# Kernel optimization log

Measured on AMD Instinct MI355X. Metric: run time of the kernel, lower is better.

Reference implementation:

```python
import jax, jax.numpy as jnp
import numpy as np

B, C, H, W, P, D, NH = 16, 3, 512, 512, 16, 128, 4
GH, GW = H // P, W // P
NP_ = GH * GW            # 1024 total patches
PD = C * P * P           # 768 patch dim
NV = NP_ // 4            # 256 visible tokens (mask_ratio = 0.75)
ENC_L, DEC_L = 6, 2
FF = 4 * D

def layer_norm(x, w, b, eps=1e-5):
    m = jnp.mean(x, -1, keepdims=True)
    v = jnp.mean((x - m) ** 2, -1, keepdims=True)
    return (x - m) * jax.lax.rsqrt(v + eps) * w + b

def mha(x, qkv_w, qkv_b, out_w, out_b):
    Bq, S, Dm = x.shape
    hd = Dm // NH
    q, k, v = jnp.split(x @ qkv_w.T + qkv_b, 3, axis=-1)
    sh = lambda t: t.reshape(Bq, S, NH, hd).transpose(0, 2, 1, 3)
    q, k, v = sh(q), sh(k), sh(v)
    scale = jnp.asarray(1.0 / np.sqrt(hd), x.dtype)
    att = jax.nn.softmax(jnp.einsum('bhqd,bhkd->bhqk', q, k) * scale, axis=-1)
    o = jnp.einsum('bhqk,bhkd->bhqd', att, v).transpose(0, 2, 1, 3).reshape(Bq, S, Dm)
    return o @ out_w.T + out_b

def stack(x, qkv_w, qkv_b, out_w, out_b, ln1_w, ln1_b, ff1_w, ff1_b, ff2_w, ff2_b, ln2_w, ln2_b):
    # post-norm nn.TransformerEncoderLayer, eval mode (dropout off), exact gelu
    for i in range(qkv_w.shape[0]):
        x = layer_norm(x + mha(x, qkv_w[i], qkv_b[i], out_w[i], out_b[i]), ln1_w[i], ln1_b[i])
        h = jax.nn.gelu(x @ ff1_w[i].T + ff1_b[i], approximate=False) @ ff2_w[i].T + ff2_b[i]
        x = layer_norm(x + h, ln2_w[i], ln2_b[i])
    return x

def setup_inputs():
    key = jax.random.key(0)
    ks = iter(jax.random.split(key, 64))
    f = lambda *s: jax.random.normal(next(ks), s, jnp.float32) * 0.02
    inp = {
        'x': jax.random.normal(next(ks), (B, C, H, W), jnp.float32),
        'vis_idx': jax.vmap(lambda k: jax.random.permutation(k, NP_))(jax.random.split(next(ks), B))[:, :NV].astype(jnp.int32),
        'w_patch': f(D, PD), 'b_patch': jnp.zeros((D,), jnp.float32),
        'mask_token': f(1, D), 'pos_embed': f(1, NP_, D),
        'w_recon': f(PD, D), 'b_recon': jnp.zeros((PD,), jnp.float32),
    }
    for pre, L in (('enc', ENC_L), ('dec', DEC_L)):
        inp[pre + '_qkv_w'] = f(L, 3 * D, D)
        inp[pre + '_qkv_b'] = jnp.zeros((L, 3 * D), jnp.float32)
        inp[pre + '_out_w'] = f(L, D, D)
        inp[pre + '_out_b'] = jnp.zeros((L, D), jnp.float32)
        inp[pre + '_ln1_w'] = jnp.ones((L, D), jnp.float32)
        inp[pre + '_ln1_b'] = jnp.zeros((L, D), jnp.float32)
        inp[pre + '_ff1_w'] = f(L, FF, D)
        inp[pre + '_ff1_b'] = jnp.zeros((L, FF), jnp.float32)
        inp[pre + '_ff2_w'] = f(L, D, FF)
        inp[pre + '_ff2_b'] = jnp.zeros((L, D), jnp.float32)
        inp[pre + '_ln2_w'] = jnp.ones((L, D), jnp.float32)
        inp[pre + '_ln2_b'] = jnp.zeros((L, D), jnp.float32)
    return inp

def reference(x, vis_idx, w_patch, b_patch, mask_token, pos_embed, w_recon, b_recon,
              enc_qkv_w, enc_qkv_b, enc_out_w, enc_out_b, enc_ln1_w, enc_ln1_b,
              enc_ff1_w, enc_ff1_b, enc_ff2_w, enc_ff2_b, enc_ln2_w, enc_ln2_b,
              dec_qkv_w, dec_qkv_b, dec_out_w, dec_out_b, dec_ln1_w, dec_ln1_b,
              dec_ff1_w, dec_ff1_b, dec_ff2_w, dec_ff2_b, dec_ln2_w, dec_ln2_b):
    # patchify: matches nn.Unfold(kernel=stride=P) channel-major patch layout
    patches = x.reshape(B, C, GH, P, GW, P).transpose(0, 2, 4, 1, 3, 5).reshape(B, NP_, PD)
    tok = patches @ w_patch.T + b_patch                    # [B, NP, D]
    bidx = jnp.arange(B)[:, None]
    vis = tok[bidx, vis_idx]                               # [B, NV, D] packed visible tokens
    enc = stack(vis, enc_qkv_w, enc_qkv_b, enc_out_w, enc_out_b, enc_ln1_w, enc_ln1_b,
                enc_ff1_w, enc_ff1_b, enc_ff2_w, enc_ff2_b, enc_ln2_w, enc_ln2_b)
    # mask_token everywhere, scatter encoded tokens back to their positions
    full = jnp.broadcast_to(mask_token, (B, NP_, D)).at[bidx, vis_idx].set(enc)
    full = full + pos_embed
    dec = stack(full, dec_qkv_w, dec_qkv_b, dec_out_w, dec_out_b, dec_ln1_w, dec_ln1_b,
                dec_ff1_w, dec_ff1_b, dec_ff2_w, dec_ff2_b, dec_ln2_w, dec_ln2_b)
    rec = dec @ w_recon.T + b_recon                        # [B, NP, PD]
    # unpatchify: [B,GH,GW,C,P,P] -> permute(0,3,1,4,2,5) -> [B,C,H,W]
    img = rec.reshape(B, GH, GW, C, P, P).transpose(0, 3, 1, 4, 2, 5).reshape(B, C, H, W)
    return img
```

## Files before the change

kernel.cpp:

```cpp
#include <hip/hip_runtime.h>
#include <math.h>

typedef unsigned short ushort_t;
typedef __attribute__((ext_vector_type(8))) short bf16x8;
typedef __attribute__((ext_vector_type(4))) float f32x4;
typedef __attribute__((ext_vector_type(16))) float f32x16;
typedef __attribute__((ext_vector_type(2))) unsigned uint2v;

__device__ __forceinline__ ushort_t f2bf(float f){
  union{float f; unsigned u;} v; v.f = f;
  unsigned r = v.u + 0x7FFFu + ((v.u >> 16) & 1u);
  return (ushort_t)(r >> 16);
}
__device__ __forceinline__ float bf2f(ushort_t h){
  union{unsigned u; float f;} v; v.u = ((unsigned)h) << 16; return v.f;
}
__device__ __forceinline__ float gelu_exact(float v){
  return 0.5f * v * (1.f + erff(v * 0.70710678118654752f));
}
#define GLD16(gp, lp) __builtin_amdgcn_global_load_lds( \
    (const __attribute__((address_space(1))) void*)(gp), \
    (__attribute__((address_space(3))) void*)(lp), 16, 0, 0)

static __device__ __forceinline__ f32x4 mfma16(bf16x8 a, bf16x8 b, f32x4 c){
  return __builtin_amdgcn_mfma_f32_16x16x32_bf16(a, b, c, 0, 0, 0);
}
static __device__ __forceinline__ f32x16 mfma32(bf16x8 a, bf16x8 b, f32x16 c){
  return __builtin_amdgcn_mfma_f32_32x32x16_bf16(a, b, c, 0, 0, 0);
}

template<int BT, int MI, int SRC, int EPI>
__global__ __launch_bounds__(256) void mfma_gemm(
    const ushort_t* __restrict__ A, const ushort_t* __restrict__ W,
    const float* __restrict__ bias, void* __restrict__ Cout,
    int M, int N, int K, ushort_t* __restrict__ vT, int slog, float qs)
{
  __shared__ ushort_t smem[BT*64 + BT*64];
  ushort_t* Al = smem;
  ushort_t* Wl = smem + BT*64;
  const int tid = threadIdx.x;
  const int lane = tid & 63, w = tid >> 6;
  const int wr = w >> 1, wc = w & 1;
  const int g = lane >> 4, lq = lane & 15;
  const int m0 = blockIdx.y * BT, n0 = blockIdx.x * BT;

  const f32x4 zf = {0.f, 0.f, 0.f, 0.f};
  f32x4 acc[MI][MI];
#pragma unroll
  for (int i = 0; i < MI; ++i)
#pragma unroll
    for (int j = 0; j < MI; ++j) acc[i][j] = zf;

  float bv[MI];
#pragma unroll
  for (int ni = 0; ni < MI; ++ni) bv[ni] = bias[n0 + wc*(BT/2) + ni*16 + lq];

  const int KT = K >> 6;
  for (int kt = 0; kt < KT; ++kt) {
    if (kt) __syncthreads();
    const int k0 = kt << 6;
#pragma unroll
    for (int i = 0; i < BT/32; ++i) {
      int chunk = i*256 + tid;
      int row = chunk >> 3, c = chunk & 7;
      int kk = k0 + ((c ^ (row & 7)) << 3);
      const ushort_t* src;
      if (SRC == 0) {
        src = A + (size_t)(m0 + row) * K + kk;
      } else {
        int gm = m0 + row;
        int bb = gm >> 10, pp = gm & 1023, gh = pp >> 5, gw = pp & 31;
        int ci = kk >> 8, rem = kk & 255, py = rem >> 4, px = rem & 15;
        src = A + ((size_t)((bb*3 + ci)*512 + gh*16 + py) * 512 + gw*16 + px);
      }
      GLD16(src, (char*)Al + chunk*16);
    }
#pragma unroll
    for (int i = 0; i < BT/32; ++i) {
      int chunk = i*256 + tid;
      int row = chunk >> 3, c = chunk & 7;
      int kk = k0 + ((c ^ (row & 7)) << 3);
      GLD16(W + (size_t)(n0 + row) * K + kk, (char*)Wl + chunk*16);
    }
    __syncthreads();
#pragma unroll
    for (int ks = 0; ks < 2; ++ks) {
      bf16x8 af[MI], bfr[MI];
#pragma unroll
      for (int mi = 0; mi < MI; ++mi) {
        int row = wr*(BT/2) + mi*16 + lq;
        int c = (ks*4 + g) ^ (row & 7);
        af[mi] = *(const bf16x8*)((const char*)Al + row*128 + c*16);
      }
#pragma unroll
      for (int ni = 0; ni < MI; ++ni) {
        int row = wc*(BT/2) + ni*16 + lq;
        int c = (ks*4 + g) ^ (row & 7);
        bfr[ni] = *(const bf16x8*)((const char*)Wl + row*128 + c*16);
      }
#pragma unroll
      for (int mi = 0; mi < MI; ++mi)
#pragma unroll
        for (int ni = 0; ni < MI; ++ni)
          acc[mi][ni] = mfma16(af[mi], bfr[ni], acc[mi][ni]);
    }
  }

  if (EPI == 3 && n0 >= 256) {
    const int Sm1 = (1 << slog) - 1;
#pragma unroll
    for (int mi = 0; mi < MI; ++mi) {
      int gm0 = m0 + wr*(BT/2) + mi*16 + g*4;
      int bb = gm0 >> slog, s0 = gm0 & Sm1;
#pragma unroll
      for (int ni = 0; ni < MI; ++ni) {
        int n = n0 + wc*(BT/2) + ni*16 + lq;
        int vcol = n - 256, hh = vcol >> 5, dd = vcol & 31;
        unsigned pw0 = ((unsigned)f2bf(acc[mi][ni][0] + bv[ni])) |
                       (((unsigned)f2bf(acc[mi][ni][1] + bv[ni])) << 16);
        unsigned pw1 = ((unsigned)f2bf(acc[mi][ni][2] + bv[ni])) |
                       (((unsigned)f2bf(acc[mi][ni][3] + bv[ni])) << 16);
        uint2 pk; pk.x = pw0; pk.y = pw1;
        *(uint2*)(vT + (((size_t)(bb*4 + hh)*32 + dd) << slog) + s0) = pk;
      }
    }
    return;
  }

  if (EPI == 2) {
    float* img = (float*)Cout;
#pragma unroll
    for (int mi = 0; mi < MI; ++mi) {
#pragma unroll
      for (int r = 0; r < 4; ++r) {
        int gm = m0 + wr*(BT/2) + mi*16 + g*4 + r;
        int bb = gm >> 10, pp = gm & 1023, gh = pp >> 5, gw = pp & 31;
#pragma unroll
        for (int ni = 0; ni < MI; ++ni) {
          int n = n0 + wc*(BT/2) + ni*16 + lq;
          int ci = n >> 8, rem = n & 255, py = rem >> 4, px = rem & 15;
          img[(size_t)((bb*3 + ci)*512 + gh*16 + py)*512 + gw*16 + px] =
              acc[mi][ni][r] + bv[ni];
        }
      }
    }
  } else {
    const float cs = (EPI == 3 && n0 < 128) ? qs : 1.0f;
    __syncthreads();
    constexpr int CPR = BT/8;
#pragma unroll
    for (int mi = 0; mi < MI; ++mi)
#pragma unroll
      for (int ni = 0; ni < MI; ++ni)
#pragma unroll
        for (int r = 0; r < 4; ++r) {
          int row = wr*(BT/2) + mi*16 + g*4 + r;
          int col = wc*(BT/2) + ni*16 + lq;
          float v = acc[mi][ni][r] + bv[ni];
          if (EPI == 3) v *= cs;
          int cc = (col >> 3) ^ (row & (CPR-1));
          smem[row*BT + cc*8 + (col & 7)] = f2bf(v);
        }
    __syncthreads();
    ushort_t* Co = (ushort_t*)Cout;
#pragma unroll
    for (int i = 0; i < BT*BT/2048; ++i) {
      int chunk = i*256 + tid;
      int row = chunk / CPR, cc = chunk % CPR;
      int c = cc ^ (row & (CPR-1));
      bf16x8 v = *(const bf16x8*)((const char*)smem + chunk*16);
      *(bf16x8*)(Co + (size_t)(m0+row)*N + n0 + c*8) = v;
    }
  }
}

template<int MI2, int QKV>
__global__ __launch_bounds__(512, 4) void mega8(
    const ushort_t* __restrict__ Ao, const ushort_t* __restrict__ Wo,
    const float* __restrict__ bo, ushort_t* __restrict__ X,
    const float* __restrict__ l1w, const float* __restrict__ l1b,
    const ushort_t* __restrict__ W1, const float* __restrict__ b1,
    const ushort_t* __restrict__ W2, const float* __restrict__ b2,
    const float* __restrict__ l2w, const float* __restrict__ l2b,
    const ushort_t* __restrict__ Wq, const float* __restrict__ bq,
    ushort_t* __restrict__ qkvb, ushort_t* __restrict__ vT,
    int slog, float qs)
{
  constexpr int BM = MI2 * 16;
  constexpr int TB = BM * 128;
  __shared__ __align__(16) ushort_t Xl[2*BM*64];
  __shared__ __align__(16) ushort_t Hl[8*BM*64];
  __shared__ __align__(16) float red[2][BM][8];
  const int tid = threadIdx.x, lane = tid & 63, w = tid >> 6;
  const int g = lane >> 4, lq = lane & 15;
  const int m0 = blockIdx.x * BM;
  const int col0 = w*16 + lq;
  const f32x4 zf = {0.f,0.f,0.f,0.f};

  f32x4 acc[MI2];
#pragma unroll
  for (int mi = 0; mi < MI2; ++mi) acc[mi] = zf;
  {
    bf16x8 a1[MI2][4], bo8[4];
#pragma unroll
    for (int mi = 0; mi < MI2; ++mi)
#pragma unroll
      for (int kf = 0; kf < 4; ++kf)
        a1[mi][kf] = *(const bf16x8*)(Ao + (size_t)(m0 + mi*16 + lq)*128 + kf*32 + g*8);
#pragma unroll
    for (int kf = 0; kf < 4; ++kf)
      bo8[kf] = *(const bf16x8*)(Wo + (size_t)col0*128 + kf*32 + g*8);
#pragma unroll
    for (int kf = 0; kf < 4; ++kf)
#pragma unroll
      for (int mi = 0; mi < MI2; ++mi)
        acc[mi] = mfma16(a1[mi][kf], bo8[kf], acc[mi]);
  }

  float xp[MI2][4];
  {
    const float bv = bo[col0], lwv = l1w[col0], lbv = l1b[col0];
#pragma unroll
    for (int mi = 0; mi < MI2; ++mi)
#pragma unroll
      for (int r = 0; r < 4; ++r) {
        int row = m0 + mi*16 + g*4 + r;
        float v = acc[mi][r] + bv + bf2f(X[(size_t)row*128 + col0]);
        xp[mi][r] = v;
        float s = v, q = v*v;
        s += __shfl_xor(s,1); s += __shfl_xor(s,2); s += __shfl_xor(s,4); s += __shfl_xor(s,8);
        q += __shfl_xor(q,1); q += __shfl_xor(q,2); q += __shfl_xor(q,4); q += __shfl_xor(q,8);
        if (lq == 0) { red[0][mi*16+g*4+r][w] = s; red[1][mi*16+g*4+r][w] = q; }
      }
    __syncthreads();
#pragma unroll
    for (int mi = 0; mi < MI2; ++mi)
#pragma unroll
      for (int r = 0; r < 4; ++r) {
        int rl = mi*16 + g*4 + r;
        float4 s0 = *(const float4*)&red[0][rl][0], s1 = *(const float4*)&red[0][rl][4];
        float4 q0 = *(const float4*)&red[1][rl][0], q1 = *(const float4*)&red[1][rl][4];
        float s = s0.x+s0.y+s0.z+s0.w + s1.x+s1.y+s1.z+s1.w;
        float q = q0.x+q0.y+q0.z+q0.w + q1.x+q1.y+q1.z+q1.w;
        float mean = s * 0.0078125f;
        float var = q * 0.0078125f - mean*mean;
        float rstd = rsqrtf(var + 1e-5f);
        float val = (xp[mi][r]-mean)*rstd*lwv + lbv;
        xp[mi][r] = val;
        ushort_t hv = f2bf(val);
        X[(size_t)(m0+rl)*128 + col0] = hv;
        int kt = col0 >> 6, c8 = (col0 & 63) >> 3, he = col0 & 7;
        *(ushort_t*)((char*)Xl + kt*TB + rl*128 + ((c8 ^ (rl & 7)) << 4) + he*2) = hv;
      }
  }
  __syncthreads();

  bf16x8 a2[MI2][4];
#pragma unroll
  for (int mi = 0; mi < MI2; ++mi)
#pragma unroll
    for (int kf = 0; kf < 4; ++kf) {
      int kt = kf >> 1, row = mi*16 + lq;
      int c = ((kf & 1)*4 + g) ^ (row & 7);
      a2[mi][kf] = *(const bf16x8*)((const char*)Xl + kt*TB + row*128 + c*16);
    }

#pragma unroll
  for (int hp = 0; hp < 4; ++hp) {
    const int hid = hp*128 + col0;
    bf16x8 b18[4];
#pragma unroll
    for (int kf = 0; kf < 4; ++kf)
      b18[kf] = *(const bf16x8*)(W1 + (size_t)hid*128 + kf*32 + g*8);
    f32x4 acc1[MI2];
#pragma unroll
    for (int mi = 0; mi < MI2; ++mi) acc1[mi] = zf;
#pragma unroll
    for (int kf = 0; kf < 4; ++kf)
#pragma unroll
      for (int mi = 0; mi < MI2; ++mi)
        acc1[mi] = mfma16(a2[mi][kf], b18[kf], acc1[mi]);
    const float bb = b1[hid];
    const int hkt = hid >> 6, hc8 = (hid & 63) >> 3, he = hid & 7;
#pragma unroll
    for (int mi = 0; mi < MI2; ++mi)
#pragma unroll
      for (int r = 0; r < 4; ++r) {
        int mrow = mi*16 + g*4 + r;
        float hv = gelu_exact(acc1[mi][r] + bb);
        *(ushort_t*)((char*)Hl + hkt*TB + mrow*128 + ((hc8 ^ (mrow & 7)) << 4) + he*2) = f2bf(hv);
      }
  }
  __syncthreads();

  f32x4 acc2[MI2];
#pragma unroll
  for (int mi = 0; mi < MI2; ++mi) acc2[mi] = zf;
#pragma unroll
  for (int kf = 0; kf < 16; ++kf) {
    int kt = kf >> 1;
    bf16x8 af[MI2], bfr;
#pragma unroll
    for (int mi = 0; mi < MI2; ++mi) {
      int row = mi*16 + lq;
      int c = ((kf & 1)*4 + g) ^ (row & 7);
      af[mi] = *(const bf16x8*)((const char*)Hl + kt*TB + row*128 + c*16);
    }
    bfr = *(const bf16x8*)(W2 + (size_t)col0*512 + kf*32 + g*8);
#pragma unroll
    for (int mi = 0; mi < MI2; ++mi)
      acc2[mi] = mfma16(af[mi], bfr, acc2[mi]);
  }

  {
    const float bv = b2[col0], lwv = l2w[col0], lbv = l2b[col0];
#pragma unroll
    for (int mi = 0; mi < MI2; ++mi)
#pragma unroll
      for (int r = 0; r < 4; ++r) {
        float v = acc2[mi][r] + bv + xp[mi][r];
        xp[mi][r] = v;
        float s = v, q = v*v;
        s += __shfl_xor(s,1); s += __shfl_xor(s,2); s += __shfl_xor(s,4); s += __shfl_xor(s,8);
        q += __shfl_xor(q,1); q += __shfl_xor(q,2); q += __shfl_xor(q,4); q += __shfl_xor(q,8);
        if (lq == 0) { red[0][mi*16+g*4+r][w] = s; red[1][mi*16+g*4+r][w] = q; }
      }
    __syncthreads();
#pragma unroll
    for (int mi = 0; mi < MI2; ++mi)
#pragma unroll
      for (int r = 0; r < 4; ++r) {
        int rl = mi*16 + g*4 + r;
        float4 s0 = *(const float4*)&red[0][rl][0], s1 = *(const float4*)&red[0][rl][4];
        float4 q0 = *(const float4*)&red[1][rl][0], q1 = *(const float4*)&red[1][rl][4];
        float s = s0.x+s0.y+s0.z+s0.w + s1.x+s1.y+s1.z+s1.w;
        float q = q0.x+q0.y+q0.z+q0.w + q1.x+q1.y+q1.z+q1.w;
        float mean = s * 0.0078125f;
        float var = q * 0.0078125f - mean*mean;
        float rstd = rsqrtf(var + 1e-5f);
        float val = (xp[mi][r]-mean)*rstd*lwv + lbv;
        ushort_t hv = f2bf(val);
        X[(size_t)(m0+rl)*128 + col0] = hv;
        if (QKV) {
          int kt = col0 >> 6, c8 = (col0 & 63) >> 3, he = col0 & 7;
          *(ushort_t*)((char*)Xl + kt*TB + rl*128 + ((c8 ^ (rl & 7)) << 4) + he*2) = hv;
        }
      }
  }

  if (QKV) {
    __syncthreads();
    bf16x8 a3[MI2][4];
#pragma unroll
    for (int mi = 0; mi < MI2; ++mi)
#pragma unroll
      for (int kf = 0; kf < 4; ++kf) {
        int kt = kf >> 1, row = mi*16 + lq;
        int c = ((kf & 1)*4 + g) ^ (row & 7);
        a3[mi][kf] = *(const bf16x8*)((const char*)Xl + kt*TB + row*128 + c*16);
      }
    const int Sm1 = (1 << slog) - 1;
#pragma unroll
    for (int pp = 0; pp < 3; ++pp) {
      const int colq = pp*128 + col0;
      bf16x8 bq8[4];
#pragma unroll
      for (int kf = 0; kf < 4; ++kf)
        bq8[kf] = *(const bf16x8*)(Wq + (size_t)colq*128 + kf*32 + g*8);
      f32x4 aq[MI2];
#pragma unroll
      for (int mi = 0; mi < MI2; ++mi) aq[mi] = zf;
#pragma unroll
      for (int kf = 0; kf < 4; ++kf)
#pragma unroll
        for (int mi = 0; mi < MI2; ++mi)
          aq[mi] = mfma16(a3[mi][kf], bq8[kf], aq[mi]);
      const float bias = bq[colq];
      if (pp < 2) {
        const float sc = (pp == 0) ? qs : 1.f;
#pragma unroll
        for (int mi = 0; mi < MI2; ++mi)
#pragma unroll
          for (int r = 0; r < 4; ++r) {
            int row = m0 + mi*16 + g*4 + r;
            qkvb[(size_t)row*384 + colq] = f2bf((aq[mi][r] + bias)*sc);
          }
      } else {
        const int hh = col0 >> 5, dd = col0 & 31;
#pragma unroll
        for (int mi = 0; mi < MI2; ++mi) {
          int gm0 = m0 + mi*16 + g*4;
          int bb = gm0 >> slog, s0 = gm0 & Sm1;
          unsigned pw0 = ((unsigned)f2bf(aq[mi][0] + bias)) |
                         (((unsigned)f2bf(aq[mi][1] + bias)) << 16);
          unsigned pw1 = ((unsigned)f2bf(aq[mi][2] + bias)) |
                         (((unsigned)f2bf(aq[mi][3] + bias)) << 16);
          uint2 pk; pk.x = pw0; pk.y = pw1;
          *(uint2*)(vT + (((size_t)(bb*4 + hh)*32 + dd) << slog) + s0) = pk;
        }
      }
    }
  }
}

template<int S, int JS>
__global__ __launch_bounds__(256) void attn32(
    const ushort_t* __restrict__ qkv, const ushort_t* __restrict__ vTg,
    ushort_t* __restrict__ o)
{
  constexpr int LDSB = (JS == 1) ? 16384 : 32768;
  __shared__ __align__(16) char smem[LDSB];
  const int tid = threadIdx.x, lane = tid & 63, w = tid >> 6;
  const int hi = lane >> 5, lq = lane & 31;
  int lin = blockIdx.x;
  int nid = (lin & 7) * 64 + (lin >> 3);
  int bx = nid & 7, bh = nid >> 3;
  int h = bh & 3, b = bh >> 2;
  const int q0 = (JS == 1) ? (bx*128 + w*32) : (bx*32);

  bf16x8 bq0 = *(const bf16x8*)(qkv + (size_t)(b*S + q0 + lq)*384 + h*32 + hi*8);
  bf16x8 bq1 = *(const bf16x8*)(qkv + (size_t)(b*S + q0 + lq)*384 + h*32 + 16 + hi*8);

  f32x16 O;
#pragma unroll
  for (int i = 0; i < 16; ++i) O[i] = 0.f;
  const f32x16 z16 = O;
  float l = 0.f;

  auto stageK = [&](char* Kb, int j0, int ci){
    int k = ci >> 2, cp = ci & 3, c = cp ^ (k & 3);
    GLD16(qkv + (size_t)(b*S + j0 + k)*384 + 128 + h*32 + c*8, Kb + ci*16);
  };
  auto stageV = [&](char* Vb, int j0, int ci){
    int d = ci >> 3, cp = ci & 7, c = cp ^ (d & 7);
    GLD16(vTg + (size_t)(bh*32 + d)*S + j0 + c*8, Vb + ci*16);
  };

  auto sm_pack = [&](const f32x16& stv, unsigned* wd){
    float p[16];
#pragma unroll
    for (int r = 0; r < 16; ++r) { p[r] = __expf(stv[r]); l += p[r]; }
#pragma unroll
    for (int i = 0; i < 8; ++i) {
      unsigned u0 = __float_as_uint(p[2*i])   + 0x8000u;
      unsigned u1 = __float_as_uint(p[2*i+1]) + 0x8000u;
      wd[i] = (u0 >> 16) | (u1 & 0xFFFF0000u);
    }
  };
  auto pvstep = [&](unsigned* wd, const char* Vb, int mt){
    uint2v s02 = __builtin_amdgcn_permlane32_swap(wd[0], wd[2], false, false);
    uint2v s13 = __builtin_amdgcn_permlane32_swap(wd[1], wd[3], false, false);
    uint2v s46 = __builtin_amdgcn_permlane32_swap(wd[4], wd[6], false, false);
    uint2v s57 = __builtin_amdgcn_permlane32_swap(wd[5], wd[7], false, false);
    union { unsigned u[4]; bf16x8 v; } pa0, pa1;
    pa0.u[0] = s02[0]; pa0.u[1] = s13[0]; pa0.u[2] = s02[1]; pa0.u[3] = s13[1];
    pa1.u[0] = s46[0]; pa1.u[1] = s57[0]; pa1.u[2] = s46[1]; pa1.u[3] = s57[1];
    int d = lq;
    bf16x8 v0 = *(const bf16x8*)(Vb + d*128 + (((mt*4 + hi)     ^ (d & 7)) << 4));
    bf16x8 v1 = *(const bf16x8*)(Vb + d*128 + (((mt*4 + 2 + hi) ^ (d & 7)) << 4));
    O = mfma32(pa0.v, v0, O);
    O = mfma32(pa1.v, v1, O);
  };
  auto computeTile = [&](const char* Kb, const char* Vb){
    const int k0 = lq, k1 = 32 + lq;
    bf16x8 a00 = *(const bf16x8*)(Kb + k0*64 + (((hi)     ^ (k0 & 3)) << 4));
    bf16x8 a01 = *(const bf16x8*)(Kb + k0*64 + (((2 + hi) ^ (k0 & 3)) << 4));
    f32x16 st0 = mfma32(a00, bq0, z16);
    st0 = mfma32(a01, bq1, st0);
    bf16x8 a10 = *(const bf16x8*)(Kb + k1*64 + (((hi)     ^ (k1 & 3)) << 4));
    bf16x8 a11 = *(const bf16x8*)(Kb + k1*64 + (((2 + hi) ^ (k1 & 3)) << 4));
    f32x16 st1 = mfma32(a10, bq0, z16);
    st1 = mfma32(a11, bq1, st1);
    unsigned wd0[8], wd1[8];
    sm_pack(st0, wd0);
    sm_pack(st1, wd1);
    pvstep(wd0, Vb, 0);
    pvstep(wd1, Vb, 1);
  };

  if (JS == 4) {
    char* Kb = smem + w*8192;
    char* Vb = Kb + 4096;
    const int j0 = w*64;
#pragma unroll
    for (int i = 0; i < 4; ++i) stageK(Kb, j0, i*64 + lane);
#pragma unroll
    for (int i = 0; i < 4; ++i) stageV(Vb, j0, i*64 + lane);
    __syncthreads();
    computeTile(Kb, Vb);
    float lw = l + __shfl_xor(l, 32);
    __syncthreads();
    float* F = (float*)smem;
#pragma unroll
    for (int r = 0; r < 16; ++r) F[(w*16 + r)*64 + lane] = O[r];
    if (hi == 0) F[4096 + w*32 + lq] = lw;
    __syncthreads();
    if (w == 0) {
      float lt = F[4096 + lq] + F[4096 + 32 + lq] + F[4096 + 64 + lq] + F[4096 + 96 + lq];
      float linv = 1.f / lt;
#pragma unroll
      for (int r = 0; r < 16; ++r) {
        float s = F[r*64 + lane] + F[(16 + r)*64 + lane] +
                  F[(32 + r)*64 + lane] + F[(48 + r)*64 + lane];
        int qr = (r & 3) + 8*(r >> 2) + 4*hi;
        float li = __shfl(linv, qr);
        o[(size_t)(b*S + q0 + qr)*128 + h*32 + lq] = f2bf(s*li);
      }
    }
  } else {
    char* K0 = smem, *V0 = smem + 4096, *K1 = smem + 8192, *V1 = smem + 12288;
    stageK(K0, 0, tid);
    stageV(V0, 0, tid);
    const int NT = S/64;
    for (int t = 0; t < NT; ++t) {
      __syncthreads();
      if (t + 1 < NT) {
        char* Kb = (t & 1) ? K0 : K1;
        char* Vb = (t & 1) ? V0 : V1;
        stageK(Kb, (t + 1)*64, tid);
        stageV(Vb, (t + 1)*64, tid);
      }
      computeTile((t & 1) ? K1 : K0, (t & 1) ? V1 : V0);
    }
    float ltot = l + __shfl_xor(l, 32);
    float linv = 1.f / ltot;
#pragma unroll
    for (int r = 0; r < 16; ++r) {
      int qr = (r & 3) + 8*(r >> 2) + 4*hi;
      float li = __shfl(linv, qr);
      o[(size_t)(b*S + q0 + qr)*128 + h*32 + lq] = f2bf(O[r]*li);
    }
  }
}

struct CastArgs {
  const float* src[11];
  ushort_t* dst[11];
  int start[11];
};
__global__ __launch_bounds__(256) void cast_all(CastArgs a, int total8){
  int i = blockIdx.x*256 + threadIdx.x;
  if (i >= total8) return;
  int s = 0;
#pragma unroll
  for (int k = 1; k < 11; ++k) if (i >= a.start[k]) s = k;
  int off = (i - a.start[s]) * 8;
  const float* sp = a.src[s] + off;
  float4 f0 = *(const float4*)sp;
  float4 f1 = *(const float4*)(sp + 4);
  bf16x8 r;
  r[0]=(short)f2bf(f0.x); r[1]=(short)f2bf(f0.y); r[2]=(short)f2bf(f0.z); r[3]=(short)f2bf(f0.w);
  r[4]=(short)f2bf(f1.x); r[5]=(short)f2bf(f1.y); r[6]=(short)f2bf(f1.z); r[7]=(short)f2bf(f1.w);
  *(bf16x8*)(a.dst[s] + off) = r;
}

__global__ __launch_bounds__(256) void gather_k(const ushort_t* __restrict__ tok,
    const int* __restrict__ vis, ushort_t* __restrict__ xe){
  int i = blockIdx.x*256 + threadIdx.x;
  int r = i >> 4, e = (i & 15)*8;
  int b = r >> 8;
  int p = vis[r];
  *(bf16x8*)(xe + (size_t)r*128 + e) = *(const bf16x8*)(tok + ((size_t)b*1024 + p)*128 + e);
}

__global__ __launch_bounds__(256) void fill_k(const float* __restrict__ mask_tok,
    const float* __restrict__ pos, ushort_t* __restrict__ full){
  int i = blockIdx.x*256 + threadIdx.x;
  int off0 = i*8;
  int d = off0 & 127;
  int p = (off0 >> 7) & 1023;
  float4 m0 = *(const float4*)(mask_tok + d);
  float4 m1 = *(const float4*)(mask_tok + d + 4);
  const float* pp = pos + (size_t)p*128 + d;
  float4 p0 = *(const float4*)pp, p1 = *(const float4*)(pp + 4);
  bf16x8 r;
  r[0]=(short)f2bf(m0.x+p0.x); r[1]=(short)f2bf(m0.y+p0.y);
  r[2]=(short)f2bf(m0.z+p0.z); r[3]=(short)f2bf(m0.w+p0.w);
  r[4]=(short)f2bf(m1.x+p1.x); r[5]=(short)f2bf(m1.y+p1.y);
  r[6]=(short)f2bf(m1.z+p1.z); r[7]=(short)f2bf(m1.w+p1.w);
  *(bf16x8*)(full + off0) = r;
}

__global__ __launch_bounds__(256) void scatter_k(const ushort_t* __restrict__ enc,
    const int* __restrict__ vis, const float* __restrict__ pos, ushort_t* __restrict__ full){
  int i = blockIdx.x*256 + threadIdx.x;
  int r = i >> 4, e = (i & 15)*8;
  int b = r >> 8;
  int p = vis[r];
  bf16x8 ev = *(const bf16x8*)(enc + (size_t)r*128 + e);
  const float* pp = pos + (size_t)p*128 + e;
  float4 p0 = *(const float4*)pp, p1 = *(const float4*)(pp + 4);
  bf16x8 out;
  out[0]=(short)f2bf(bf2f((ushort_t)ev[0]) + p0.x);
  out[1]=(short)f2bf(bf2f((ushort_t)ev[1]) + p0.y);
  out[2]=(short)f2bf(bf2f((ushort_t)ev[2]) + p0.z);
  out[3]=(short)f2bf(bf2f((ushort_t)ev[3]) + p0.w);
  out[4]=(short)f2bf(bf2f((ushort_t)ev[4]) + p1.x);
  out[5]=(short)f2bf(bf2f((ushort_t)ev[5]) + p1.y);
  out[6]=(short)f2bf(bf2f((ushort_t)ev[6]) + p1.z);
  out[7]=(short)f2bf(bf2f((ushort_t)ev[7]) + p1.w);
  *(bf16x8*)(full + ((size_t)b*1024 + p)*128 + e) = out;
}

extern "C" void kernel_launch(void* const* d_in, const int* in_sizes, int n_in,
                              void* d_out, int out_size, void* d_ws, size_t ws_size,
                              hipStream_t stream)
{
  const float* x        = (const float*)d_in[0];
  const int*   vis      = (const int*)d_in[1];
  const float* b_patch  = (const float*)d_in[3];
  const float* mask_tok = (const float*)d_in[4];
  const float* pos      = (const float*)d_in[5];
  const float* b_recon  = (const float*)d_in[7];
  float* out = (float*)d_out;
  const float QS = 0.17677669529663687f;

  ushort_t* ws    = (ushort_t*)d_ws;
  ushort_t* tok   = ws;
  ushort_t* xe    = tok  + 2097152;
  ushort_t* qkvb  = xe   + 524288;
  ushort_t* obuf  = qkvb + 8388608;
  ushort_t* tbuf  = obuf + 2097152;
  ushort_t* xbf   = tbuf + 2097152;
  ushort_t* wbf   = xbf  + 12582912;

  ushort_t* w_qkv_e = wbf;
  ushort_t* w_out_e = w_qkv_e + 294912;
  ushort_t* w_ff1_e = w_out_e + 98304;
  ushort_t* w_ff2_e = w_ff1_e + 393216;
  ushort_t* w_qkv_d = w_ff2_e + 393216;
  ushort_t* w_out_d = w_qkv_d + 98304;
  ushort_t* w_ff1_d = w_out_d + 32768;
  ushort_t* w_ff2_d = w_ff1_d + 131072;
  ushort_t* w_pat   = w_ff2_d + 131072;
  ushort_t* w_rec   = w_pat   + 98304;
  ushort_t* vT      = w_rec   + 98304;

  CastArgs ca;
  const float* srcs[11] = {x, (const float*)d_in[8], (const float*)d_in[10],
                           (const float*)d_in[14], (const float*)d_in[16],
                           (const float*)d_in[20], (const float*)d_in[22],
                           (const float*)d_in[26], (const float*)d_in[28],
                           (const float*)d_in[2], (const float*)d_in[6]};
  ushort_t* dsts[11] = {xbf, w_qkv_e, w_out_e, w_ff1_e, w_ff2_e,
                        w_qkv_d, w_out_d, w_ff1_d, w_ff2_d, w_pat, w_rec};
  int sizes[11] = {12582912, 294912, 98304, 393216, 393216,
                   98304, 32768, 131072, 131072, 98304, 98304};
  int acc8 = 0;
  for (int k = 0; k < 11; ++k){ ca.src[k]=srcs[k]; ca.dst[k]=dsts[k]; ca.start[k]=acc8; acc8 += sizes[k]/8; }
  cast_all<<<dim3((acc8 + 255)/256), 256, 0, stream>>>(ca, acc8);

  mfma_gemm<64,2,1,0><<<dim3(2,256), 256, 0, stream>>>(xbf, w_pat, b_patch, tok, 16384, 128, 768, nullptr, 0, 1.f);
  gather_k<<<dim3(256), 256, 0, stream>>>(tok, vis, xe);

  mfma_gemm<64,2,0,3><<<dim3(6,64), 256, 0, stream>>>(xe, w_qkv_e, (const float*)d_in[9], qkvb, 4096, 384, 128, vT, 8, QS);
  for (int L = 0; L < 6; ++L) {
    const float* ob  = (const float*)d_in[11] + L*128;
    const float* l1w = (const float*)d_in[12] + L*128;
    const float* l1b = (const float*)d_in[13] + L*128;
    const float* f1b = (const float*)d_in[15] + L*512;
    const float* f2b = (const float*)d_in[17] + L*128;
    const float* l2w = (const float*)d_in[18] + L*128;
    const float* l2b = (const float*)d_in[19] + L*128;
    attn32<256,4><<<dim3(512), 256, 0, stream>>>(qkvb, vT, obuf);
    if (L < 5) {
      mega8<1,1><<<dim3(256), 512, 0, stream>>>(obuf, w_out_e + L*16384, ob, xe,
          l1w, l1b, w_ff1_e + L*65536, f1b, w_ff2_e + L*65536, f2b, l2w, l2b,
          w_qkv_e + (L+1)*49152, (const float*)d_in[9] + (L+1)*384, qkvb, vT, 8, QS);
    } else {
      mega8<1,0><<<dim3(256), 512, 0, stream>>>(obuf, w_out_e + L*16384, ob, xe,
          l1w, l1b, w_ff1_e + L*65536, f1b, w_ff2_e + L*65536, f2b, l2w, l2b,
          w_qkv_e, (const float*)d_in[9], qkvb, vT, 8, QS);
    }
  }

  fill_k<<<dim3(1024), 256, 0, stream>>>(mask_tok, pos, tok);
  scatter_k<<<dim3(256), 256, 0, stream>>>(xe, vis, pos, tok);

  mfma_gemm<128,4,0,3><<<dim3(3,128), 256, 0, stream>>>(tok, w_qkv_d, (const float*)d_in[21], qkvb, 16384, 384, 128, vT, 10, QS);
  for (int L = 0; L < 2; ++L) {
    const float* ob  = (const float*)d_in[23] + L*128;
    const float* l1w = (const float*)d_in[24] + L*128;
    const float* l1b = (const float*)d_in[25] + L*128;
    const float* f1b = (const float*)d_in[27] + L*512;
    const float* f2b = (const float*)d_in[29] + L*128;
    const float* l2w = (const float*)d_in[30] + L*128;
    const float* l2b = (const float*)d_in[31] + L*128;
    attn32<1024,1><<<dim3(512), 256, 0, stream>>>(qkvb, vT, obuf);
    if (L < 1) {
      mega8<2,1><<<dim3(512), 512, 0, stream>>>(obuf, w_out_d + L*16384, ob, tok,
          l1w, l1b, w_ff1_d + L*65536, f1b, w_ff2_d + L*65536, f2b, l2w, l2b,
          w_qkv_d + 49152, (const float*)d_in[21] + 384, qkvb, vT, 10, QS);
    } else {
      mega8<2,0><<<dim3(512), 512, 0, stream>>>(obuf, w_out_d + L*16384, ob, tok,
          l1w, l1b, w_ff1_d + L*65536, f1b, w_ff2_d + L*65536, f2b, l2w, l2b,
          w_qkv_d, (const float*)d_in[21], qkvb, vT, 10, QS);
    }
  }

  mfma_gemm<128,4,0,2><<<dim3(6,128), 256, 0, stream>>>(tok, w_rec, b_recon, out, 16384, 768, 128, nullptr, 0, 1.f);
}
```

Before: 330.9 us.

## Prefetch fused-layer weights into registers and use fast erf approximation

Restructures the fused out-proj/LN/FFN/LN/QKV kernel so weight fragments for W1, W2 and the next QKV projection, the residual values and the bias/LN parameters are loaded into registers ahead of use, overlapping global latency with earlier MFMA work. The residual X write after LN1 is dropped. __syncthreads is replaced by an LDS-only waitcnt plus barrier. Exact erff in GELU is swapped for an Abramowitz-Stegun polynomial with max error around 1e-7, which is cheaper but slightly changes numerics. Holding many bf16x8 fragments at once raises register pressure and may reduce occupancy or cause spills.

```diff
diff --git a/kernel.cpp b/kernel.cpp
--- a/kernel.cpp
+++ b/kernel.cpp
@@ -18,9 +18,26 @@
 __device__ __forceinline__ float gelu_exact(float v){
   return 0.5f * v * (1.f + erff(v * 0.70710678118654752f));
 }
+__device__ __forceinline__ float erf_fast(float x){
+  float ax = fabsf(x);
+  float t = 1.f / fmaf(0.3275911f, ax, 1.f);
+  float y = t*fmaf(t, fmaf(t, fmaf(t, fmaf(t, 1.061405429f, -1.453152027f),
+            1.421413741f), -0.284496736f), 0.254829592f);
+  float r = 1.f - y * __expf(-ax*ax);
+  return copysignf(r, x);
+}
+__device__ __forceinline__ float gelu_fast(float v){
+  return 0.5f * v * (1.f + erf_fast(v * 0.70710678118654752f));
+}
 #define GLD16(gp, lp) __builtin_amdgcn_global_load_lds( \
     (const __attribute__((address_space(1))) void*)(gp), \
     (__attribute__((address_space(3))) void*)(lp), 16, 0, 0)
+
+#define BAR_LDS() do { \
+  asm volatile("s_waitcnt lgkmcnt(0)" ::: "memory"); \
+  __builtin_amdgcn_s_barrier(); \
+  asm volatile("" ::: "memory"); \
+} while (0)
 
 static __device__ __forceinline__ f32x4 mfma16(bf16x8 a, bf16x8 b, f32x4 c){
   return __builtin_amdgcn_mfma_f32_16x16x32_bf16(a, b, c, 0, 0, 0);
@@ -197,63 +214,79 @@
   const int col0 = w*16 + lq;
   const f32x4 zf = {0.f,0.f,0.f,0.f};
 
+  bf16x8 a1[MI2][4], bo8[4];
+#pragma unroll
+  for (int mi = 0; mi < MI2; ++mi)
+#pragma unroll
+    for (int kf = 0; kf < 4; ++kf)
+      a1[mi][kf] = *(const bf16x8*)(Ao + (size_t)(m0 + mi*16 + lq)*128 + kf*32 + g*8);
+#pragma unroll
+  for (int kf = 0; kf < 4; ++kf)
+    bo8[kf] = *(const bf16x8*)(Wo + (size_t)col0*128 + kf*32 + g*8);
+  ushort_t rsv[MI2][4];
+#pragma unroll
+  for (int mi = 0; mi < MI2; ++mi)
+#pragma unroll
+    for (int r = 0; r < 4; ++r)
+      rsv[mi][r] = X[(size_t)(m0 + mi*16 + g*4 + r)*128 + col0];
+  bf16x8 w1p[4][4];
+#pragma unroll
+  for (int hp = 0; hp < 2; ++hp)
+#pragma unroll
+    for (int kf = 0; kf < 4; ++kf)
+      w1p[hp][kf] = *(const bf16x8*)(W1 + (size_t)(hp*128 + col0)*128 + kf*32 + g*8);
+  const float bo_v = bo[col0], l1w_v = l1w[col0], l1b_v = l1b[col0];
+  const float b2_v = b2[col0], l2w_v = l2w[col0], l2b_v = l2b[col0];
+  float b1_v[4];
+#pragma unroll
+  for (int hp = 0; hp < 4; ++hp) b1_v[hp] = b1[hp*128 + col0];
+
   f32x4 acc[MI2];
 #pragma unroll
   for (int mi = 0; mi < MI2; ++mi) acc[mi] = zf;
-  {
-    bf16x8 a1[MI2][4], bo8[4];
+#pragma unroll
+  for (int kf = 0; kf < 4; ++kf)
 #pragma unroll
     for (int mi = 0; mi < MI2; ++mi)
-#pragma unroll
-      for (int kf = 0; kf < 4; ++kf)
-        a1[mi][kf] = *(const bf16x8*)(Ao + (size_t)(m0 + mi*16 + lq)*128 + kf*32 + g*8);
+      acc[mi] = mfma16(a1[mi][kf], bo8[kf], acc[mi]);
+
+#pragma unroll
+  for (int hp = 2; hp < 4; ++hp)
 #pragma unroll
     for (int kf = 0; kf < 4; ++kf)
-      bo8[kf] = *(const bf16x8*)(Wo + (size_t)col0*128 + kf*32 + g*8);
-#pragma unroll
-    for (int kf = 0; kf < 4; ++kf)
-#pragma unroll
-      for (int mi = 0; mi < MI2; ++mi)
-        acc[mi] = mfma16(a1[mi][kf], bo8[kf], acc[mi]);
-  }
+      w1p[hp][kf] = *(const bf16x8*)(W1 + (size_t)(hp*128 + col0)*128 + kf*32 + g*8);
 
   float xp[MI2][4];
-  {
-    const float bv = bo[col0], lwv = l1w[col0], lbv = l1b[col0];
-#pragma unroll
-    for (int mi = 0; mi < MI2; ++mi)
-#pragma unroll
-      for (int r = 0; r < 4; ++r) {
-        int row = m0 + mi*16 + g*4 + r;
-        float v = acc[mi][r] + bv + bf2f(X[(size_t)row*128 + col0]);
-        xp[mi][r] = v;
-        float s = v, q = v*v;
-        s += __shfl_xor(s,1); s += __shfl_xor(s,2); s += __shfl_xor(s,4); s += __shfl_xor(s,8);
-        q += __shfl_xor(q,1); q += __shfl_xor(q,2); q += __shfl_xor(q,4); q += __shfl_xor(q,8);
-        if (lq == 0) { red[0][mi*16+g*4+r][w] = s; red[1][mi*16+g*4+r][w] = q; }
-      }
-    __syncthreads();
-#pragma unroll
-    for (int mi = 0; mi < MI2; ++mi)
-#pragma unroll
-      for (int r = 0; r < 4; ++r) {
-        int rl = mi*16 + g*4 + r;
-        float4 s0 = *(const float4*)&red[0][rl][0], s1 = *(const float4*)&red[0][rl][4];
-        float4 q0 = *(const float4*)&red[1][rl][0], q1 = *(const float4*)&red[1][rl][4];
-        float s = s0.x+s0.y+s0.z+s0.w + s1.x+s1.y+s1.z+s1.w;
-        float q = q0.x+q0.y+q0.z+q0.w + q1.x+q1.y+q1.z+q1.w;
-        float mean = s * 0.0078125f;
-        float var = q * 0.0078125f - mean*mean;
-        float rstd = rsqrtf(var + 1e-5f);
-        float val = (xp[mi][r]-mean)*rstd*lwv + lbv;
-        xp[mi][r] = val;
-        ushort_t hv = f2bf(val);
-        X[(size_t)(m0+rl)*128 + col0] = hv;
-        int kt = col0 >> 6, c8 = (col0 & 63) >> 3, he = col0 & 7;
-        *(ushort_t*)((char*)Xl + kt*TB + rl*128 + ((c8 ^ (rl & 7)) << 4) + he*2) = hv;
-      }
-  }
-  __syncthreads();
+#pragma unroll
+  for (int mi = 0; mi < MI2; ++mi)
+#pragma unroll
+    for (int r = 0; r < 4; ++r) {
+      float v = acc[mi][r] + bo_v + bf2f(rsv[mi][r]);
+      xp[mi][r] = v;
+      float s = v, q = v*v;
+      s += __shfl_xor(s,1); s += __shfl_xor(s,2); s += __shfl_xor(s,4); s += __shfl_xor(s,8);
+      q += __shfl_xor(q,1); q += __shfl_xor(q,2); q += __shfl_xor(q,4); q += __shfl_xor(q,8);
+      if (lq == 0) { red[0][mi*16+g*4+r][w] = s; red[1][mi*16+g*4+r][w] = q; }
+    }
+  BAR_LDS();
+#pragma unroll
+  for (int mi = 0; mi < MI2; ++mi)
+#pragma unroll
+    for (int r = 0; r < 4; ++r) {
+      int rl = mi*16 + g*4 + r;
+      float4 s0 = *(const float4*)&red[0][rl][0], s1 = *(const float4*)&red[0][rl][4];
+      float4 q0 = *(const float4*)&red[1][rl][0], q1 = *(const float4*)&red[1][rl][4];
+      float s = s0.x+s0.y+s0.z+s0.w + s1.x+s1.y+s1.z+s1.w;
+      float q = q0.x+q0.y+q0.z+q0.w + q1.x+q1.y+q1.z+q1.w;
+      float mean = s * 0.0078125f;
+      float var = q * 0.0078125f - mean*mean;
+      float rstd = rsqrtf(var + 1e-5f);
+      float val = (xp[mi][r]-mean)*rstd*l1w_v + l1b_v;
+      xp[mi][r] = val;
+      int kt = col0 >> 6, c8 = (col0 & 63) >> 3, he = col0 & 7;
+      *(ushort_t*)((char*)Xl + kt*TB + rl*128 + ((c8 ^ (rl & 7)) << 4) + he*2) = f2bf(val);
+    }
+  BAR_LDS();
 
   bf16x8 a2[MI2][4];
 #pragma unroll
@@ -265,91 +298,102 @@
       a2[mi][kf] = *(const bf16x8*)((const char*)Xl + kt*TB + row*128 + c*16);
     }
 
+  bf16x8 w2p[16];
 #pragma unroll
   for (int hp = 0; hp < 4; ++hp) {
+    f32x4 acc1[MI2];
+#pragma unroll
+    for (int mi = 0; mi < MI2; ++mi) acc1[mi] = zf;
+#pragma unroll
+    for (int kf = 0; kf < 4; ++kf)
+#pragma unroll
+      for (int mi = 0; mi < MI2; ++mi)
+        acc1[mi] = mfma16(a2[mi][kf], w1p[hp][kf], acc1[mi]);
+#pragma unroll
+    for (int j = 0; j < 4; ++j)
+      w2p[hp*4 + j] = *(const bf16x8*)(W2 + (size_t)col0*512 + (hp*4 + j)*32 + g*8);
     const int hid = hp*128 + col0;
-    bf16x8 b18[4];
-#pragma unroll
-    for (int kf = 0; kf < 4; ++kf)
-      b18[kf] = *(const bf16x8*)(W1 + (size_t)hid*128 + kf*32 + g*8);
-    f32x4 acc1[MI2];
-#pragma unroll
-    for (int mi = 0; mi < MI2; ++mi) acc1[mi] = zf;
-#pragma unroll
-    for (int kf = 0; kf < 4; ++kf)
-#pragma unroll
-      for (int mi = 0; mi < MI2; ++mi)
-        acc1[mi] = mfma16(a2[mi][kf], b18[kf], acc1[mi]);
-    const float bb = b1[hid];
     const int hkt = hid >> 6, hc8 = (hid & 63) >> 3, he = hid & 7;
 #pragma unroll
     for (int mi = 0; mi < MI2; ++mi)
 #pragma unroll
       for (int r = 0; r < 4; ++r) {
         int mrow = mi*16 + g*4 + r;
-        float hv = gelu_exact(acc1[mi][r] + bb);
+        float hv = gelu_fast(acc1[mi][r] + b1_v[hp]);
         *(ushort_t*)((char*)Hl + hkt*TB + mrow*128 + ((hc8 ^ (mrow & 7)) << 4) + he*2) = f2bf(hv);
       }
   }
-  __syncthreads();
-
+  BAR_LDS();
+
+  bf16x8 wqp[3][4];
   f32x4 acc2[MI2];
 #pragma unroll
   for (int mi = 0; mi < MI2; ++mi) acc2[mi] = zf;
 #pragma unroll
   for (int kf = 0; kf < 16; ++kf) {
     int kt = kf >> 1;
-    bf16x8 af[MI2], bfr;
+    bf16x8 af[MI2];
 #pragma unroll
     for (int mi = 0; mi < MI2; ++mi) {
       int row = mi*16 + lq;
       int c = ((kf & 1)*4 + g) ^ (row & 7);
       af[mi] = *(const bf16x8*)((const char*)Hl + kt*TB + row*128 + c*16);
     }
-    bfr = *(const bf16x8*)(W2 + (size_t)col0*512 + kf*32 + g*8);
 #pragma unroll
     for (int mi = 0; mi < MI2; ++mi)
-      acc2[mi] = mfma16(af[mi], bfr, acc2[mi]);
-  }
-
-  {
-    const float bv = b2[col0], lwv = l2w[col0], lbv = l2b[col0];
-#pragma unroll
-    for (int mi = 0; mi < MI2; ++mi)
-#pragma unroll
-      for (int r = 0; r < 4; ++r) {
-        float v = acc2[mi][r] + bv + xp[mi][r];
-        xp[mi][r] = v;
-        float s = v, q = v*v;
-        s += __shfl_xor(s,1); s += __shfl_xor(s,2); s += __shfl_xor(s,4); s += __shfl_xor(s,8);
-        q += __shfl_xor(q,1); q += __shfl_xor(q,2); q += __shfl_xor(q,4); q += __shfl_xor(q,8);
-        if (lq == 0) { red[0][mi*16+g*4+r][w] = s; red[1][mi*16+g*4+r][w] = q; }
-      }
-    __syncthreads();
-#pragma unroll
-    for (int mi = 0; mi < MI2; ++mi)
-#pragma unroll
-      for (int r = 0; r < 4; ++r) {
-        int rl = mi*16 + g*4 + r;
-        float4 s0 = *(const float4*)&red[0][rl][0], s1 = *(const float4*)&red[0][rl][4];
-        float4 q0 = *(const float4*)&red[1][rl][0], q1 = *(const float4*)&red[1][rl][4];
-        float s = s0.x+s0.y+s0.z+s0.w + s1.x+s1.y+s1.z+s1.w;
-        float q = q0.x+q0.y+q0.z+q0.w + q1.x+q1.y+q1.z+q1.w;
-        float mean = s * 0.0078125f;
-        float var = q * 0.0078125f - mean*mean;
-        float rstd = rsqrtf(var + 1e-5f);
-        float val = (xp[mi][r]-mean)*rstd*lwv + lbv;
-        ushort_t hv = f2bf(val);
-        X[(size_t)(m0+rl)*128 + col0] = hv;
-        if (QKV) {
-          int kt = col0 >> 6, c8 = (col0 & 63) >> 3, he = col0 & 7;
-          *(ushort_t*)((char*)Xl + kt*TB + rl*128 + ((c8 ^ (rl & 7)) << 4) + he*2) = hv;
-        }
-      }
-  }
+      acc2[mi] = mfma16(af[mi], w2p[kf], acc2[mi]);
+    if (QKV && kf == 7) {
+#pragma unroll
+      for (int j = 0; j < 4; ++j)
+        wqp[0][j] = *(const bf16x8*)(Wq + (size_t)(0*128 + col0)*128 + j*32 + g*8);
+    }
+    if (QKV && kf == 11) {
+#pragma unroll
+      for (int j = 0; j < 4; ++j)
+        wqp[1][j] = *(const bf16x8*)(Wq + (size_t)(1*128 + col0)*128 + j*32 + g*8);
+    }
+    if (QKV && kf == 15) {
+#pragma unroll
+      for (int j = 0; j < 4; ++j)
+        wqp[2][j] = *(const bf16x8*)(Wq + (size_t)(2*128 + col0)*128 + j*32 + g*8);
+    }
+  }
+
+#pragma unroll
+  for (int mi = 0; mi < MI2; ++mi)
+#pragma unroll
+    for (int r = 0; r < 4; ++r) {
+      float v = acc2[mi][r] + b2_v + xp[mi][r];
+      xp[mi][r] = v;
+      float s = v, q = v*v;
+      s += __shfl_xor(s,1); s += __shfl_xor(s,2); s += __shfl_xor(s,4); s += __shfl_xor(s,8);
+      q += __shfl_xor(q,1); q += __shfl_xor(q,2); q += __shfl_xor(q,4); q += __shfl_xor(q,8);
+      if (lq == 0) { red[0][mi*16+g*4+r][w] = s; red[1][mi*16+g*4+r][w] = q; }
+    }
+  BAR_LDS();
+#pragma unroll
+  for (int mi = 0; mi < MI2; ++mi)
+#pragma unroll
+    for (int r = 0; r < 4; ++r) {
+      int rl = mi*16 + g*4 + r;
+      float4 s0 = *(const float4*)&red[0][rl][0], s1 = *(const float4*)&red[0][rl][4];
+      float4 q0 = *(const float4*)&red[1][rl][0], q1 = *(const float4*)&red[1][rl][4];
+      float s = s0.x+s0.y+s0.z+s0.w + s1.x+s1.y+s1.z+s1.w;
+      float q = q0.x+q0.y+q0.z+q0.w + q1.x+q1.y+q1.z+q1.w;
+      float mean = s * 0.0078125f;
+      float var = q * 0.0078125f - mean*mean;
+      float rstd = rsqrtf(var + 1e-5f);
+      float val = (xp[mi][r]-mean)*rstd*l2w_v + l2b_v;
+      ushort_t hv = f2bf(val);
+      X[(size_t)(m0+rl)*128 + col0] = hv;
+      if (QKV) {
+        int kt = col0 >> 6, c8 = (col0 & 63) >> 3, he = col0 & 7;
+        *(ushort_t*)((char*)Xl + kt*TB + rl*128 + ((c8 ^ (rl & 7)) << 4) + he*2) = hv;
+      }
+    }
 
   if (QKV) {
-    __syncthreads();
+    BAR_LDS();
     bf16x8 a3[MI2][4];
 #pragma unroll
     for (int mi = 0; mi < MI2; ++mi)
@@ -363,18 +407,14 @@
 #pragma unroll
     for (int pp = 0; pp < 3; ++pp) {
       const int colq = pp*128 + col0;
-      bf16x8 bq8[4];
+      f32x4 aq[MI2];
+#pragma unroll
+      for (int mi = 0; mi < MI2; ++mi) aq[mi] = zf;
 #pragma unroll
       for (int kf = 0; kf < 4; ++kf)
-        bq8[kf] = *(const bf16x8*)(Wq + (size_t)colq*128 + kf*32 + g*8);
-      f32x4 aq[MI2];
-#pragma unroll
-      for (int mi = 0; mi < MI2; ++mi) aq[mi] = zf;
-#pragma unroll
-      for (int kf = 0; kf < 4; ++kf)
 #pragma unroll
         for (int mi = 0; mi < MI2; ++mi)
-          aq[mi] = mfma16(a3[mi][kf], bq8[kf], aq[mi]);
+          aq[mi] = mfma16(a3[mi][kf], wqp[pp][kf], aq[mi]);
       const float bias = bq[colq];
       if (pp < 2) {
         const float sc = (pp == 0) ? qs : 1.f;
```

Measured after the change: 351.4 us. 1.06x slower.

## Split decoder attention keys across waves, fast erf GELU, smaller decoder tiles

Applied to the files above, without the earlier changes.

Attention is rewritten so each of the four waves processes its own subset of key tiles and the partial outputs are reduced through LDS, now used for both encoder and decoder with 2048 decoder blocks instead of a double-buffered per-block loop. The decoder fused layer kernel switches to smaller row tiles with twice the blocks. Exact erf in GELU is replaced by a polynomial approximation using a fast exp, and a redundant global store of the post-LN1 activations is dropped. The approximation changes numerics slightly, and the per-wave staging waits on vmcnt without overlapping loads and compute.

```diff
diff --git a/kernel.cpp b/kernel.cpp
--- a/kernel.cpp
+++ b/kernel.cpp
@@ -15,8 +15,16 @@
 __device__ __forceinline__ float bf2f(ushort_t h){
   union{unsigned u; float f;} v; v.u = ((unsigned)h) << 16; return v.f;
 }
-__device__ __forceinline__ float gelu_exact(float v){
-  return 0.5f * v * (1.f + erff(v * 0.70710678118654752f));
+__device__ __forceinline__ float erf_fast(float x){
+  float ax = fabsf(x);
+  float t = 1.f / fmaf(0.3275911f, ax, 1.f);
+  float y = t*fmaf(t, fmaf(t, fmaf(t, fmaf(t, 1.061405429f, -1.453152027f),
+            1.421413741f), -0.284496736f), 0.254829592f);
+  float r = 1.f - y * __expf(-ax*ax);
+  return copysignf(r, x);
+}
+__device__ __forceinline__ float gelu_fast(float v){
+  return 0.5f * v * (1.f + erf_fast(v * 0.70710678118654752f));
 }
 #define GLD16(gp, lp) __builtin_amdgcn_global_load_lds( \
     (const __attribute__((address_space(1))) void*)(gp), \
@@ -247,10 +255,8 @@
         float rstd = rsqrtf(var + 1e-5f);
         float val = (xp[mi][r]-mean)*rstd*lwv + lbv;
         xp[mi][r] = val;
-        ushort_t hv = f2bf(val);
-        X[(size_t)(m0+rl)*128 + col0] = hv;
         int kt = col0 >> 6, c8 = (col0 & 63) >> 3, he = col0 & 7;
-        *(ushort_t*)((char*)Xl + kt*TB + rl*128 + ((c8 ^ (rl & 7)) << 4) + he*2) = hv;
+        *(ushort_t*)((char*)Xl + kt*TB + rl*128 + ((c8 ^ (rl & 7)) << 4) + he*2) = f2bf(val);
       }
   }
   __syncthreads();
@@ -287,7 +293,7 @@
 #pragma unroll
       for (int r = 0; r < 4; ++r) {
         int mrow = mi*16 + g*4 + r;
-        float hv = gelu_exact(acc1[mi][r] + bb);
+        float hv = gelu_fast(acc1[mi][r] + bb);
         *(ushort_t*)((char*)Hl + hkt*TB + mrow*128 + ((hc8 ^ (mrow & 7)) << 4) + he*2) = f2bf(hv);
       }
   }
@@ -403,20 +409,21 @@
   }
 }
 
-template<int S, int JS>
-__global__ __launch_bounds__(256) void attn32(
+template<int S, int NTW>
+__global__ __launch_bounds__(256) void attn32s(
     const ushort_t* __restrict__ qkv, const ushort_t* __restrict__ vTg,
     ushort_t* __restrict__ o)
 {
-  constexpr int LDSB = (JS == 1) ? 16384 : 32768;
-  __shared__ __align__(16) char smem[LDSB];
+  __shared__ __align__(16) char smem[32768];
   const int tid = threadIdx.x, lane = tid & 63, w = tid >> 6;
   const int hi = lane >> 5, lq = lane & 31;
+  constexpr int QB = S/32;
+  constexpr int NBLK = QB*64;
   int lin = blockIdx.x;
-  int nid = (lin & 7) * 64 + (lin >> 3);
-  int bx = nid & 7, bh = nid >> 3;
+  int nid = (lin & 7)*(NBLK/8) + (lin >> 3);
+  int bx = nid % QB, bh = nid / QB;
   int h = bh & 3, b = bh >> 2;
-  const int q0 = (JS == 1) ? (bx*128 + w*32) : (bx*32);
+  const int q0 = bx*32;
 
   bf16x8 bq0 = *(const bf16x8*)(qkv + (size_t)(b*S + q0 + lq)*384 + h*32 + hi*8);
   bf16x8 bq1 = *(const bf16x8*)(qkv + (size_t)(b*S + q0 + lq)*384 + h*32 + 16 + hi*8);
@@ -427,15 +434,17 @@
   const f32x16 z16 = O;
   float l = 0.f;
 
-  auto stageK = [&](char* Kb, int j0, int ci){
+  char* Kb = smem + w*8192;
+  char* Vb = Kb + 4096;
+
+  auto stageK = [&](int j0, int ci){
     int k = ci >> 2, cp = ci & 3, c = cp ^ (k & 3);
     GLD16(qkv + (size_t)(b*S + j0 + k)*384 + 128 + h*32 + c*8, Kb + ci*16);
   };
-  auto stageV = [&](char* Vb, int j0, int ci){
+  auto stageV = [&](int j0, int ci){
     int d = ci >> 3, cp = ci & 7, c = cp ^ (d & 7);
     GLD16(vTg + (size_t)(bh*32 + d)*S + j0 + c*8, Vb + ci*16);
   };
-
   auto sm_pack = [&](const f32x16& stv, unsigned* wd){
     float p[16];
 #pragma unroll
@@ -447,7 +456,7 @@
       wd[i] = (u0 >> 16) | (u1 & 0xFFFF0000u);
     }
   };
-  auto pvstep = [&](unsigned* wd, const char* Vb, int mt){
+  auto pvstep = [&](unsigned* wd, int mt){
     uint2v s02 = __builtin_amdgcn_permlane32_swap(wd[0], wd[2], false, false);
     uint2v s13 = __builtin_amdgcn_permlane32_swap(wd[1], wd[3], false, false);
     uint2v s46 = __builtin_amdgcn_permlane32_swap(wd[4], wd[6], false, false);
@@ -461,7 +470,7 @@
     O = mfma32(pa0.v, v0, O);
     O = mfma32(pa1.v, v1, O);
   };
-  auto computeTile = [&](const char* Kb, const char* Vb){
+  auto computeTile = [&](){
     const int k0 = lq, k1 = 32 + lq;
     bf16x8 a00 = *(const bf16x8*)(Kb + k0*64 + (((hi)     ^ (k0 & 3)) << 4));
     bf16x8 a01 = *(const bf16x8*)(Kb + k0*64 + (((2 + hi) ^ (k0 & 3)) << 4));
@@ -474,61 +483,40 @@
     unsigned wd0[8], wd1[8];
     sm_pack(st0, wd0);
     sm_pack(st1, wd1);
-    pvstep(wd0, Vb, 0);
-    pvstep(wd1, Vb, 1);
+    pvstep(wd0, 0);
+    pvstep(wd1, 1);
   };
 
-  if (JS == 4) {
-    char* Kb = smem + w*8192;
-    char* Vb = Kb + 4096;
-    const int j0 = w*64;
-#pragma unroll
-    for (int i = 0; i < 4; ++i) stageK(Kb, j0, i*64 + lane);
-#pragma unroll
-    for (int i = 0; i < 4; ++i) stageV(Vb, j0, i*64 + lane);
-    __syncthreads();
-    computeTile(Kb, Vb);
-    float lw = l + __shfl_xor(l, 32);
-    __syncthreads();
-    float* F = (float*)smem;
-#pragma unroll
-    for (int r = 0; r < 16; ++r) F[(w*16 + r)*64 + lane] = O[r];
-    if (hi == 0) F[4096 + w*32 + lq] = lw;
-    __syncthreads();
-    if (w == 0) {
-      float lt = F[4096 + lq] + F[4096 + 32 + lq] + F[4096 + 64 + lq] + F[4096 + 96 + lq];
-      float linv = 1.f / lt;
-#pragma unroll
-      for (int r = 0; r < 16; ++r) {
-        float s = F[r*64 + lane] + F[(16 + r)*64 + lane] +
-                  F[(32 + r)*64 + lane] + F[(48 + r)*64 + lane];
-        int qr = (r & 3) + 8*(r >> 2) + 4*hi;
-        float li = __shfl(linv, qr);
-        o[(size_t)(b*S + q0 + qr)*128 + h*32 + lq] = f2bf(s*li);
-      }
-    }
-  } else {
-    char* K0 = smem, *V0 = smem + 4096, *K1 = smem + 8192, *V1 = smem + 12288;
-    stageK(K0, 0, tid);
-    stageV(V0, 0, tid);
-    const int NT = S/64;
-    for (int t = 0; t < NT; ++t) {
-      __syncthreads();
-      if (t + 1 < NT) {
-        char* Kb = (t & 1) ? K0 : K1;
-        char* Vb = (t & 1) ? V0 : V1;
-        stageK(Kb, (t + 1)*64, tid);
-        stageV(Vb, (t + 1)*64, tid);
-      }
-      computeTile((t & 1) ? K1 : K0, (t & 1) ? V1 : V0);
-    }
-    float ltot = l + __shfl_xor(l, 32);
-    float linv = 1.f / ltot;
+#pragma unroll
+  for (int i = 0; i < NTW; ++i) {
+    const int j0 = (w + 4*i)*64;
+#pragma unroll
+    for (int c = 0; c < 4; ++c) stageK(j0, c*64 + lane);
+#pragma unroll
+    for (int c = 0; c < 4; ++c) stageV(j0, c*64 + lane);
+    asm volatile("s_waitcnt vmcnt(0)" ::: "memory");
+    __builtin_amdgcn_sched_barrier(0);
+    computeTile();
+    asm volatile("" ::: "memory");
+  }
+
+  float lw = l + __shfl_xor(l, 32);
+  __syncthreads();
+  float* F = (float*)smem;
+#pragma unroll
+  for (int r = 0; r < 16; ++r) F[(w*16 + r)*64 + lane] = O[r];
+  if (hi == 0) F[4096 + w*32 + lq] = lw;
+  __syncthreads();
+  if (w == 0) {
+    float lt = F[4096 + lq] + F[4096 + 32 + lq] + F[4096 + 64 + lq] + F[4096 + 96 + lq];
+    float linv = 1.f / lt;
 #pragma unroll
     for (int r = 0; r < 16; ++r) {
+      float s = F[r*64 + lane] + F[(16 + r)*64 + lane] +
+                F[(32 + r)*64 + lane] + F[(48 + r)*64 + lane];
       int qr = (r & 3) + 8*(r >> 2) + 4*hi;
       float li = __shfl(linv, qr);
-      o[(size_t)(b*S + q0 + qr)*128 + h*32 + lq] = f2bf(O[r]*li);
+      o[(size_t)(b*S + q0 + qr)*128 + h*32 + lq] = f2bf(s*li);
     }
   }
 }
@@ -662,7 +650,7 @@
     const float* f2b = (const float*)d_in[17] + L*128;
     const float* l2w = (const float*)d_in[18] + L*128;
     const float* l2b = (const float*)d_in[19] + L*128;
-    attn32<256,4><<<dim3(512), 256, 0, stream>>>(qkvb, vT, obuf);
+    attn32s<256,1><<<dim3(512), 256, 0, stream>>>(qkvb, vT, obuf);
     if (L < 5) {
       mega8<1,1><<<dim3(256), 512, 0, stream>>>(obuf, w_out_e + L*16384, ob, xe,
           l1w, l1b, w_ff1_e + L*65536, f1b, w_ff2_e + L*65536, f2b, l2w, l2b,
@@ -686,13 +674,13 @@
     const float* f2b = (const float*)d_in[29] + L*128;
     const float* l2w = (const float*)d_in[30] + L*128;
     const float* l2b = (const float*)d_in[31] + L*128;
-    attn32<1024,1><<<dim3(512), 256, 0, stream>>>(qkvb, vT, obuf);
+    attn32s<1024,4><<<dim3(2048), 256, 0, stream>>>(qkvb, vT, obuf);
     if (L < 1) {
-      mega8<2,1><<<dim3(512), 512, 0, stream>>>(obuf, w_out_d + L*16384, ob, tok,
+      mega8<1,1><<<dim3(1024), 512, 0, stream>>>(obuf, w_out_d + L*16384, ob, tok,
           l1w, l1b, w_ff1_d + L*65536, f1b, w_ff2_d + L*65536, f2b, l2w, l2b,
           w_qkv_d + 49152, (const float*)d_in[21] + 384, qkvb, vT, 10, QS);
     } else {
-      mega8<2,0><<<dim3(512), 512, 0, stream>>>(obuf, w_out_d + L*16384, ob, tok,
+      mega8<1,0><<<dim3(1024), 512, 0, stream>>>(obuf, w_out_d + L*16384, ob, tok,
           l1w, l1b, w_ff1_d + L*65536, f1b, w_ff2_d + L*65536, f2b, l2w, l2b,
           w_qkv_d, (const float*)d_in[21], qkvb, vT, 10, QS);
     }
```

Measured after the change: 362.3 us. +9.5%, slower.
